# Performance work log

Hardware: AMD Instinct MI355X
Metric: run time of the kernel (lower is better)

## Reference

```python
import jax, jax.numpy as jnp
import numpy as np

DIM = 1024
HEADS = 16
HEAD_DIM = DIM // HEADS
BLOCK = 32
FEAT = 128
EPS = 1e-8


def setup_inputs() -> dict:
    key = jax.random.key(0)
    ks = jax.random.split(key, 5)
    b, n = 4, 4096
    x = jax.random.normal(ks[0], (b, n, DIM), dtype=jnp.float32)
    Wqkv = jax.random.normal(ks[1], (DIM, 3 * DIM), dtype=jnp.float32) / np.sqrt(DIM)
    proj = jax.random.normal(ks[2], (HEADS, HEAD_DIM, FEAT), dtype=jnp.float32) / np.sqrt(HEAD_DIM)
    Wout = jax.random.normal(ks[3], (DIM, DIM), dtype=jnp.float32) / np.sqrt(DIM)
    bout = jnp.zeros((DIM,), dtype=jnp.float32)
    return {"x": x, "Wqkv": Wqkv, "proj": proj, "Wout": Wout, "bout": bout}


def reference(x, Wqkv, proj, Wout, bout):
    b, n, d = x.shape
    h, dh = HEADS, HEAD_DIM
    nb = n // BLOCK
    qkv = x @ Wqkv                                    # [b, n, 3d]
    q, k, v = jnp.split(qkv, 3, axis=-1)
    # [b, h, nb, bs, dh]
    def to_blocks(t):
        return t.reshape(b, nb, BLOCK, h, dh).transpose(0, 3, 1, 2, 4)
    q, k, v = to_blocks(q), to_blocks(k), to_blocks(v)
    # per-head feature projection + elu feature map
    qf = jax.nn.elu(jnp.einsum('bhmsd,hdf->bhmsf', q, proj)) + 1.0
    kf = jax.nn.elu(jnp.einsum('bhmsd,hdf->bhmsf', k, proj)) + 1.0
    kv = jnp.einsum('bhmsf,bhmsd->bhmfd', kf, v)      # per-block kv state
    out = jnp.einsum('bhmsf,bhmfd->bhmsd', qf, kv)
    z = 1.0 / (jnp.einsum('bhmsf,bhmf->bhms', qf, kf.sum(axis=3)) + EPS)
    out = out * z[..., None]
    out = out.transpose(0, 2, 3, 1, 4).reshape(b, n, d)  # [b, n, d]
    return out @ Wout + bout
```

## Files before the change

### kernel.cpp

```cpp
#include <hip/hip_runtime.h>
#include <stdint.h>


typedef unsigned short u16;
typedef __attribute__((ext_vector_type(4))) float f32x4;
typedef __attribute__((ext_vector_type(8))) __bf16 bf16x8;
typedef __attribute__((ext_vector_type(8))) u16 us8;
typedef __attribute__((ext_vector_type(4))) u16 us4;

#define GLOAD_LDS16(g, l)                                                      \
  __builtin_amdgcn_global_load_lds(                                            \
      (const __attribute__((address_space(1))) void*)(g),                      \
      (__attribute__((address_space(3))) void*)(l), 16, 0, 0)

__device__ __forceinline__ u16 f2bf(float f) {
  union { float f; unsigned u; } x; x.f = f;
  return (u16)((x.u + 0x7fffu + ((x.u >> 16) & 1u)) >> 16);
}

__device__ __forceinline__ bf16x8 ld8(const void* p) {
  return __builtin_bit_cast(bf16x8, *(const us8*)p);
}

__device__ __forceinline__ f32x4 mfma16(bf16x8 a, bf16x8 b, f32x4 c) {
  return __builtin_amdgcn_mfma_f32_16x16x32_bf16(a, b, c, 0, 0, 0);
}

__global__ void cast_bf16_k(const float* __restrict__ in, u16* __restrict__ out,
                            int n4) {
  int stride = gridDim.x * blockDim.x;
  for (int i = blockIdx.x * blockDim.x + threadIdx.x; i < n4; i += stride) {
    f32x4 v = ((const f32x4*)in)[i];
    us4 o;
    o[0] = f2bf(v[0]); o[1] = f2bf(v[1]); o[2] = f2bf(v[2]); o[3] = f2bf(v[3]);
    ((us4*)out)[i] = o;
  }
}

__global__ __launch_bounds__(256)
void tcast_k(const float* __restrict__ in, u16* __restrict__ out, int R, int C) {
  __shared__ float tile[32][33];
  int tx = threadIdx.x & 31, ty = threadIdx.x >> 5;
  int r0 = blockIdx.y * 32, c0 = blockIdx.x * 32;
#pragma unroll
  for (int i = 0; i < 32; i += 8)
    tile[ty + i][tx] = in[(size_t)(r0 + ty + i) * C + c0 + tx];
  __syncthreads();
#pragma unroll
  for (int i = 0; i < 32; i += 8)
    out[(size_t)(c0 + ty + i) * R + r0 + tx] = f2bf(tile[tx][ty + i]);
}

__global__ void pcast_k(const float* __restrict__ in, u16* __restrict__ out) {
  int idx = blockIdx.x * 256 + threadIdx.x;
  int h = idx >> 13, f = (idx >> 6) & 127, e = idx & 63;
  out[idx] = f2bf(in[h * 8192 + e * 128 + f]);
}

template <bool OUTF32>
__global__ __launch_bounds__(256)
void gemm_bt(const u16* __restrict__ A, const u16* __restrict__ Bt,
             const float* __restrict__ bias, void* __restrict__ Cv,
             int M, int N, int K) {
  __shared__ __align__(16) u16 As[128 * 32];
  __shared__ __align__(16) u16 Bs[128 * 32];
  const int tid = threadIdx.x, lane = tid & 63, wave = tid >> 6;
  const int wr = wave >> 1, wc = wave & 1;
  const int bxN = blockIdx.x * 128;
  const int byM = blockIdx.y * 128;
  const int lr = lane & 15, lg = lane >> 4;
  const int r_in = lane >> 2;
  const int kch = (lane & 3) * 8;

  f32x4 acc[4][4];
#pragma unroll
  for (int m = 0; m < 4; ++m)
#pragma unroll
    for (int n = 0; n < 4; ++n) acc[m][n] = (f32x4){0.f, 0.f, 0.f, 0.f};

  for (int kt = 0; kt < K; kt += 32) {
    __syncthreads();
#pragma unroll
    for (int c = 0; c < 2; ++c) {
      int rowA = byM + wave * 32 + c * 16 + r_in;
      int rowB = bxN + wave * 32 + c * 16 + r_in;
      GLOAD_LDS16(A + (size_t)rowA * K + kt + kch, As + (wave * 2 + c) * 512);
      GLOAD_LDS16(Bt + (size_t)rowB * K + kt + kch, Bs + (wave * 2 + c) * 512);
    }
    __syncthreads();
    bf16x8 a[4], b[4];
#pragma unroll
    for (int m = 0; m < 4; ++m)
      a[m] = ld8(&As[(wr * 64 + m * 16 + lr) * 32 + lg * 8]);
#pragma unroll
    for (int n = 0; n < 4; ++n)
      b[n] = ld8(&Bs[(wc * 64 + n * 16 + lr) * 32 + lg * 8]);
#pragma unroll
    for (int m = 0; m < 4; ++m)
#pragma unroll
      for (int n = 0; n < 4; ++n) acc[m][n] = mfma16(a[m], b[n], acc[m][n]);
  }

  const int rbase = byM + wr * 64 + lg * 4;
  const int cbase = bxN + wc * 64 + lr;
#pragma unroll
  for (int m = 0; m < 4; ++m) {
#pragma unroll
    for (int n = 0; n < 4; ++n) {
      int col = cbase + n * 16;
      float bia = OUTF32 ? bias[col] : 0.f;
#pragma unroll
      for (int r = 0; r < 4; ++r) {
        int row = rbase + m * 16 + r;
        if (OUTF32)
          ((float*)Cv)[(size_t)row * N + col] = acc[m][n][r] + bia;
        else
          ((u16*)Cv)[(size_t)row * N + col] = f2bf(acc[m][n][r]);
      }
    }
  }
}

__global__ __launch_bounds__(64)
void attn_block_k(const u16* __restrict__ qkv, const u16* __restrict__ projT,
                  u16* __restrict__ attn) {
  __shared__ __align__(16) u16 qf_l[32 * 128];
  __shared__ __align__(16) u16 kf_l[32 * 128];
  __shared__ __align__(16) u16 V_l[32 * 72];
  __shared__ __align__(16) u16 S_l[32 * 32];

  const int lane = threadIdx.x;
  const int bid = blockIdx.x;
  const int m = bid & 127, h = (bid >> 7) & 15, b = bid >> 11;
  const size_t t0 = (size_t)b * 4096 + (size_t)m * 32;
  const u16* qb = qkv + t0 * 3072 + h * 64;
  const u16* kb = qb + 1024;
  const u16* vb = qb + 2048;
  const u16* pT = projT + h * 8192;
  const int lr = lane & 15, lg = lane >> 4;

  bf16x8 bp[8][2];
#pragma unroll
  for (int f = 0; f < 8; ++f)
#pragma unroll
    for (int ks = 0; ks < 2; ++ks)
      bp[f][ks] = ld8(&pT[(f * 16 + lr) * 64 + ks * 32 + lg * 8]);

#pragma unroll
  for (int it = 0; it < 4; ++it) {
    int s = it * 8 + (lane >> 3);
    int d0 = (lane & 7) * 8;
    *(us8*)&V_l[s * 72 + d0] = *(const us8*)&vb[(size_t)s * 3072 + d0];
  }

#pragma unroll
  for (int pass = 0; pass < 2; ++pass) {
    const u16* src = pass ? kb : qb;
    u16* dst = pass ? kf_l : qf_l;
    f32x4 acc[2][8];
#pragma unroll
    for (int mm = 0; mm < 2; ++mm)
#pragma unroll
      for (int f = 0; f < 8; ++f) acc[mm][f] = (f32x4){0.f, 0.f, 0.f, 0.f};
    bf16x8 afr[2][2];
#pragma unroll
    for (int mm = 0; mm < 2; ++mm)
#pragma unroll
      for (int ks = 0; ks < 2; ++ks)
        afr[mm][ks] = ld8(&src[(size_t)(mm * 16 + lr) * 3072 + ks * 32 + lg * 8]);
#pragma unroll
    for (int mm = 0; mm < 2; ++mm)
#pragma unroll
      for (int ks = 0; ks < 2; ++ks)
#pragma unroll
        for (int f = 0; f < 8; ++f)
          acc[mm][f] = mfma16(afr[mm][ks], bp[f][ks], acc[mm][f]);
#pragma unroll
    for (int mm = 0; mm < 2; ++mm)
#pragma unroll
      for (int f = 0; f < 8; ++f)
#pragma unroll
        for (int r = 0; r < 4; ++r) {
          float x = acc[mm][f][r];
          float v = x > 0.f ? x + 1.f : __expf(x);
          int row = mm * 16 + lg * 4 + r;
          int byi = (f * 16 + lr) * 2;
          *(u16*)((char*)dst + row * 256 + (byi ^ ((row & 7) << 4))) = f2bf(v);
        }
  }

  f32x4 sacc[2][2];
#pragma unroll
  for (int mm = 0; mm < 2; ++mm)
#pragma unroll
    for (int nn = 0; nn < 2; ++nn) sacc[mm][nn] = (f32x4){0.f, 0.f, 0.f, 0.f};
#pragma unroll
  for (int ks = 0; ks < 4; ++ks) {
    int byi = (ks * 32 + lg * 8) * 2;
    bf16x8 aq[2], bk[2];
#pragma unroll
    for (int mm = 0; mm < 2; ++mm) {
      int row = mm * 16 + lr;
      aq[mm] = ld8((char*)qf_l + row * 256 + (byi ^ ((row & 7) << 4)));
      bk[mm] = ld8((char*)kf_l + row * 256 + (byi ^ ((row & 7) << 4)));
    }
#pragma unroll
    for (int mm = 0; mm < 2; ++mm)
#pragma unroll
      for (int nn = 0; nn < 2; ++nn)
        sacc[mm][nn] = mfma16(aq[mm], bk[nn], sacc[mm][nn]);
  }

  float rs[2][4];
#pragma unroll
  for (int mm = 0; mm < 2; ++mm)
#pragma unroll
    for (int r = 0; r < 4; ++r) {
      float t = sacc[mm][0][r] + sacc[mm][1][r];
      t += __shfl_xor(t, 1);
      t += __shfl_xor(t, 2);
      t += __shfl_xor(t, 4);
      t += __shfl_xor(t, 8);
      rs[mm][r] = t;
    }

#pragma unroll
  for (int mm = 0; mm < 2; ++mm)
#pragma unroll
    for (int nn = 0; nn < 2; ++nn)
#pragma unroll
      for (int r = 0; r < 4; ++r) {
        int row = mm * 16 + lg * 4 + r;
        int byi = (nn * 16 + lr) * 2;
        *(u16*)((char*)S_l + row * 64 + (byi ^ ((row & 3) << 4))) =
            f2bf(sacc[mm][nn][r]);
      }

  bf16x8 vfr[4];
#pragma unroll
  for (int nn = 0; nn < 4; ++nn) {
    us8 g;
#pragma unroll
    for (int j = 0; j < 8; ++j) g[j] = V_l[(lg * 8 + j) * 72 + nn * 16 + lr];
    vfr[nn] = __builtin_bit_cast(bf16x8, g);
  }
  f32x4 pacc[2][4];
#pragma unroll
  for (int mm = 0; mm < 2; ++mm)
#pragma unroll
    for (int nn = 0; nn < 4; ++nn) pacc[mm][nn] = (f32x4){0.f, 0.f, 0.f, 0.f};
#pragma unroll
  for (int mm = 0; mm < 2; ++mm) {
    int row = mm * 16 + lr;
    int byi = lg * 16;
    bf16x8 a = ld8((char*)S_l + row * 64 + (byi ^ ((row & 3) << 4)));
#pragma unroll
    for (int nn = 0; nn < 4; ++nn) pacc[mm][nn] = mfma16(a, vfr[nn], pacc[mm][nn]);
  }

#pragma unroll
  for (int mm = 0; mm < 2; ++mm)
#pragma unroll
    for (int r = 0; r < 4; ++r) {
      float z = 1.f / (rs[mm][r] + 1e-8f);
      int q = mm * 16 + lg * 4 + r;
#pragma unroll
      for (int nn = 0; nn < 4; ++nn)
        attn[(t0 + q) * 1024 + h * 64 + nn * 16 + lr] =
            f2bf(pacc[mm][nn][r] * z);
    }
}

extern "C" void kernel_launch(void* const* d_in, const int* in_sizes, int n_in,
                              void* d_out, int out_size, void* d_ws,
                              size_t ws_size, hipStream_t stream) {
  const float* x = (const float*)d_in[0];
  const float* Wqkv = (const float*)d_in[1];
  const float* proj = (const float*)d_in[2];
  const float* Wout = (const float*)d_in[3];
  const float* bout = (const float*)d_in[4];
  float* out = (float*)d_out;

  char* ws = (char*)d_ws;
  u16* xb    = (u16*)(ws + 0);
  u16* wqkvT = (u16*)(ws + 33554432);
  u16* qkv   = (u16*)(ws + 39845888);
  u16* projT = (u16*)(ws + 140509184);
  u16* attn  = (u16*)(ws + 140771328);
  u16* woutT = (u16*)(ws + 174325760);

  cast_bf16_k<<<2048, 256, 0, stream>>>(x, xb, (16384 * 1024) / 4);
  tcast_k<<<dim3(3072 / 32, 1024 / 32), 256, 0, stream>>>(Wqkv, wqkvT, 1024, 3072);
  tcast_k<<<dim3(1024 / 32, 1024 / 32), 256, 0, stream>>>(Wout, woutT, 1024, 1024);
  pcast_k<<<512, 256, 0, stream>>>(proj, projT);

  gemm_bt<false><<<dim3(3072 / 128, 16384 / 128), 256, 0, stream>>>(
      xb, wqkvT, nullptr, qkv, 16384, 3072, 1024);

  attn_block_k<<<8192, 64, 0, stream>>>(qkv, projT, attn);

  gemm_bt<true><<<dim3(1024 / 128, 16384 / 128), 256, 0, stream>>>(
      attn, woutT, bout, out, 16384, 1024, 1024);
}
```

Measured before the change: 389.9 us.

## Fold feature projection into QKV weights and use 256x256 pipelined GEMM

Precomputes Wq·proj and Wk·proj on device so the first GEMM directly produces the 128-wide q/k features, with the elu+1 map applied in its epilogue. The attention kernel then only does the block-local score and value products, reading features from global memory. Both GEMMs switch to a 512-thread, 256x256-tile kernel with double-buffered LDS, a swizzled layout, and interleaved loads and MFMAs. This widens the first GEMM's N from 3072 to 5120, adding FLOPs, and uses the output buffer as scratch for the staged inputs.

```diff
diff --git a/kernel.cpp b/kernel.cpp
--- a/kernel.cpp
+++ b/kernel.cpp
@@ -51,142 +51,236 @@
     out[(size_t)(c0 + ty + i) * R + r0 + tx] = f2bf(tile[tx][ty + i]);
 }
 
-__global__ void pcast_k(const float* __restrict__ in, u16* __restrict__ out) {
-  int idx = blockIdx.x * 256 + threadIdx.x;
-  int h = idx >> 13, f = (idx >> 6) & 127, e = idx & 63;
-  out[idx] = f2bf(in[h * 8192 + e * 128 + f]);
-}
-
-template <bool OUTF32>
 __global__ __launch_bounds__(256)
-void gemm_bt(const u16* __restrict__ A, const u16* __restrict__ Bt,
-             const float* __restrict__ bias, void* __restrict__ Cv,
-             int M, int N, int K) {
-  __shared__ __align__(16) u16 As[128 * 32];
-  __shared__ __align__(16) u16 Bs[128 * 32];
-  const int tid = threadIdx.x, lane = tid & 63, wave = tid >> 6;
-  const int wr = wave >> 1, wc = wave & 1;
-  const int bxN = blockIdx.x * 128;
-  const int byM = blockIdx.y * 128;
+void tcastv_k(const float* __restrict__ Wqkv, u16* __restrict__ dst) {
+  __shared__ float tile[32][33];
+  int tx = threadIdx.x & 31, ty = threadIdx.x >> 5;
+  int e0 = blockIdx.y * 32, j0 = blockIdx.x * 32;
+#pragma unroll
+  for (int i = 0; i < 32; i += 8)
+    tile[ty + i][tx] = Wqkv[(size_t)(e0 + ty + i) * 3072 + 2048 + j0 + tx];
+  __syncthreads();
+#pragma unroll
+  for (int i = 0; i < 32; i += 8)
+    dst[(size_t)(j0 + ty + i) * 1024 + e0 + tx] = f2bf(tile[tx][ty + i]);
+}
+
+__global__ __launch_bounds__(256)
+void wqpb_k(const float* __restrict__ Wqkv, const float* __restrict__ proj,
+            u16* __restrict__ BtAll) {
+  __shared__ float pl[64][128];
+  const int ec = blockIdx.x, h = blockIdx.y, qk = blockIdx.z;
+  const float* ph = proj + (size_t)h * 8192;
+  for (int i = threadIdx.x; i < 2048; i += 256)
+    ((f32x4*)&pl[0][0])[i] = ((const f32x4*)ph)[i];
+  __syncthreads();
+  const int e = ec * 128 + (threadIdx.x >> 1);
+  const int f0 = (threadIdx.x & 1) * 64;
+  float wrow[64];
+  const float* src = Wqkv + (size_t)e * 3072 + qk * 1024 + h * 64;
+#pragma unroll
+  for (int i = 0; i < 16; ++i)
+    *(f32x4*)&wrow[i * 4] = *(const f32x4*)&src[i * 4];
+  u16* dst = BtAll + (size_t)(qk * 2048 + h * 128) * 1024 + e;
+  for (int fg = 0; fg < 16; ++fg) {
+    f32x4 acc = (f32x4){0.f, 0.f, 0.f, 0.f};
+    const int f = f0 + fg * 4;
+#pragma unroll
+    for (int d = 0; d < 64; ++d) {
+      f32x4 p = *(f32x4*)&pl[d][f];
+      acc += wrow[d] * p;
+    }
+#pragma unroll
+    for (int u = 0; u < 4; ++u) dst[(size_t)(f + u) * 1024] = f2bf(acc[u]);
+  }
+}
+
+template <int EPI>
+__global__ __launch_bounds__(512, 1)
+void gemm8p_k(const u16* __restrict__ A, int lda,
+              const u16* __restrict__ Bt, int ldb,
+              const float* __restrict__ bias,
+              u16* __restrict__ o_qkf, u16* __restrict__ o_v,
+              float* __restrict__ o_f32, int K, int ntx) {
+  __shared__ __align__(16) char lds[131072];
+  const int tid = threadIdx.x, lane = tid & 63, w = tid >> 6;
+  const int wm = w >> 2, wn = w & 3;
   const int lr = lane & 15, lg = lane >> 4;
-  const int r_in = lane >> 2;
-  const int kch = (lane & 3) * 8;
-
-  f32x4 acc[4][4];
-#pragma unroll
-  for (int m = 0; m < 4; ++m)
-#pragma unroll
-    for (int n = 0; n < 4; ++n) acc[m][n] = (f32x4){0.f, 0.f, 0.f, 0.f};
-
-  for (int kt = 0; kt < K; kt += 32) {
-    __syncthreads();
-#pragma unroll
-    for (int c = 0; c < 2; ++c) {
-      int rowA = byM + wave * 32 + c * 16 + r_in;
-      int rowB = bxN + wave * 32 + c * 16 + r_in;
-      GLOAD_LDS16(A + (size_t)rowA * K + kt + kch, As + (wave * 2 + c) * 512);
-      GLOAD_LDS16(Bt + (size_t)rowB * K + kt + kch, Bs + (wave * 2 + c) * 512);
-    }
-    __syncthreads();
-    bf16x8 a[4], b[4];
-#pragma unroll
-    for (int m = 0; m < 4; ++m)
-      a[m] = ld8(&As[(wr * 64 + m * 16 + lr) * 32 + lg * 8]);
-#pragma unroll
-    for (int n = 0; n < 4; ++n)
-      b[n] = ld8(&Bs[(wc * 64 + n * 16 + lr) * 32 + lg * 8]);
-#pragma unroll
-    for (int m = 0; m < 4; ++m)
-#pragma unroll
-      for (int n = 0; n < 4; ++n) acc[m][n] = mfma16(a[m], b[n], acc[m][n]);
-  }
-
-  const int rbase = byM + wr * 64 + lg * 4;
-  const int cbase = bxN + wc * 64 + lr;
-#pragma unroll
-  for (int m = 0; m < 4; ++m) {
-#pragma unroll
-    for (int n = 0; n < 4; ++n) {
-      int col = cbase + n * 16;
-      float bia = OUTF32 ? bias[col] : 0.f;
-#pragma unroll
-      for (int r = 0; r < 4; ++r) {
-        int row = rbase + m * 16 + r;
-        if (OUTF32)
-          ((float*)Cv)[(size_t)row * N + col] = acc[m][n][r] + bia;
-        else
-          ((u16*)Cv)[(size_t)row * N + col] = f2bf(acc[m][n][r]);
-      }
-    }
-  }
+  const int cpx = (int)gridDim.x >> 3;
+  const int bid = blockIdx.x;
+  const int s = (bid & 7) * cpx + (bid >> 3);
+  const int bxN = (s % ntx) * 256;
+  const int byM = (s / ntx) * 256;
+  const int nt = K >> 6;
+
+  const int srow = w * 8 + (lane >> 3);
+  const int scol = ((lane & 7) ^ ((lane >> 3) & 7)) * 8;
+
+  auto stg = [&](const u16* src, int ld, int row0, int kt, int dstoff) {
+#pragma unroll
+    for (int j = 0; j < 2; ++j)
+      GLOAD_LDS16(src + (size_t)(row0 + j * 64 + srow) * ld + kt + scol,
+                  lds + dstoff + j * 8192 + w * 1024);
+  };
+  auto stgA0 = [&](int t) { stg(A, lda, byM, t * 64, (t & 1) * 65536); };
+  auto stgA1 = [&](int t) { stg(A, lda, byM + 128, t * 64, (t & 1) * 65536 + 16384); };
+  auto stgB0 = [&](int t) { stg(Bt, ldb, bxN, t * 64, (t & 1) * 65536 + 32768); };
+  auto stgB1 = [&](int t) { stg(Bt, ldb, bxN + 128, t * 64, (t & 1) * 65536 + 49152); };
+
+  f32x4 acc[8][4];
+#pragma unroll
+  for (int i = 0; i < 8; ++i)
+#pragma unroll
+    for (int j = 0; j < 4; ++j) acc[i][j] = (f32x4){0.f, 0.f, 0.f, 0.f};
+
+  stgA0(0); stgA1(0); stgB0(0); stgB1(0);
+  if (nt > 1) {
+    stgB0(1); stgB1(1);
+    asm volatile("s_waitcnt vmcnt(4)" ::: "memory");
+  } else {
+    asm volatile("s_waitcnt vmcnt(0)" ::: "memory");
+  }
+  __builtin_amdgcn_s_barrier();
+
+  for (int t = 0; t < nt; ++t) {
+    const char* Ab = lds + (t & 1) * 65536 + wm * 16384;
+    const char* Bb = lds + (t & 1) * 65536 + 32768 + (wn >> 1) * 16384;
+    const int brow = (wn & 1) * 64;
+    bf16x8 a2[4][2], b2[4][2];
+
+#pragma unroll
+    for (int i = 0; i < 4; ++i)
+#pragma unroll
+      for (int ks = 0; ks < 2; ++ks) {
+        int row = i * 16 + lr;
+        a2[i][ks] = ld8(Ab + row * 128 + ((ks * 64 + lg * 16) ^ ((row & 7) << 4)));
+      }
+#pragma unroll
+    for (int j = 0; j < 2; ++j)
+#pragma unroll
+      for (int ks = 0; ks < 2; ++ks) {
+        int row = brow + j * 16 + lr;
+        b2[j][ks] = ld8(Bb + row * 128 + ((ks * 64 + lg * 16) ^ ((row & 7) << 4)));
+      }
+    if (t + 1 < nt) stgA0(t + 1);
+    __builtin_amdgcn_s_barrier();
+    asm volatile("s_waitcnt lgkmcnt(0)" ::: "memory");
+    __builtin_amdgcn_sched_barrier(0);
+    __builtin_amdgcn_s_setprio(1);
+#pragma unroll
+    for (int i = 0; i < 4; ++i)
+#pragma unroll
+      for (int j = 0; j < 2; ++j)
+#pragma unroll
+        for (int ks = 0; ks < 2; ++ks)
+          acc[i][j] = mfma16(a2[i][ks], b2[j][ks], acc[i][j]);
+    __builtin_amdgcn_s_setprio(0);
+    __builtin_amdgcn_s_barrier();
+
+#pragma unroll
+    for (int j = 2; j < 4; ++j)
+#pragma unroll
+      for (int ks = 0; ks < 2; ++ks) {
+        int row = brow + j * 16 + lr;
+        b2[j][ks] = ld8(Bb + row * 128 + ((ks * 64 + lg * 16) ^ ((row & 7) << 4)));
+      }
+    if (t + 1 < nt) stgA1(t + 1);
+    __builtin_amdgcn_s_barrier();
+    asm volatile("s_waitcnt lgkmcnt(0)" ::: "memory");
+    __builtin_amdgcn_sched_barrier(0);
+    __builtin_amdgcn_s_setprio(1);
+#pragma unroll
+    for (int i = 0; i < 4; ++i)
+#pragma unroll
+      for (int j = 2; j < 4; ++j)
+#pragma unroll
+        for (int ks = 0; ks < 2; ++ks)
+          acc[i][j] = mfma16(a2[i][ks], b2[j][ks], acc[i][j]);
+    __builtin_amdgcn_s_setprio(0);
+    __builtin_amdgcn_s_barrier();
+
+#pragma unroll
+    for (int i = 0; i < 4; ++i)
+#pragma unroll
+      for (int ks = 0; ks < 2; ++ks) {
+        int row = (4 + i) * 16 + lr;
+        a2[i][ks] = ld8(Ab + row * 128 + ((ks * 64 + lg * 16) ^ ((row & 7) << 4)));
+      }
+    if (t + 2 < nt) stgB0(t + 2);
+    __builtin_amdgcn_s_barrier();
+    asm volatile("s_waitcnt lgkmcnt(0)" ::: "memory");
+    __builtin_amdgcn_sched_barrier(0);
+    __builtin_amdgcn_s_setprio(1);
+#pragma unroll
+    for (int i = 0; i < 4; ++i)
+#pragma unroll
+      for (int j = 0; j < 2; ++j)
+#pragma unroll
+        for (int ks = 0; ks < 2; ++ks)
+          acc[4 + i][j] = mfma16(a2[i][ks], b2[j][ks], acc[4 + i][j]);
+    __builtin_amdgcn_s_setprio(0);
+    __builtin_amdgcn_s_barrier();
+
+    if (t + 2 < nt) stgB1(t + 2);
+    if (t < nt - 2)
+      asm volatile("s_waitcnt vmcnt(4)" ::: "memory");
+    else
+      asm volatile("s_waitcnt vmcnt(0)" ::: "memory");
+    __builtin_amdgcn_s_barrier();
+    __builtin_amdgcn_s_setprio(1);
+#pragma unroll
+    for (int i = 0; i < 4; ++i)
+#pragma unroll
+      for (int j = 2; j < 4; ++j)
+#pragma unroll
+        for (int ks = 0; ks < 2; ++ks)
+          acc[4 + i][j] = mfma16(a2[i][ks], b2[j][ks], acc[4 + i][j]);
+    __builtin_amdgcn_s_setprio(0);
+    __builtin_amdgcn_s_barrier();
+  }
+
+  const bool doelu = (EPI == 0) && (bxN < 4096);
+#pragma unroll
+  for (int mi = 0; mi < 8; ++mi)
+#pragma unroll
+    for (int nj = 0; nj < 4; ++nj) {
+      const int col = bxN + wn * 64 + nj * 16 + lr;
+#pragma unroll
+      for (int rr = 0; rr < 4; ++rr) {
+        const int row = byM + wm * 128 + mi * 16 + lg * 4 + rr;
+        float x = acc[mi][nj][rr];
+        if (EPI == 0) {
+          if (doelu) {
+            float v = x > 0.f ? x + 1.f : __expf(x);
+            o_qkf[(size_t)row * 4096 + col] = f2bf(v);
+          } else {
+            o_v[(size_t)row * 1024 + (col - 4096)] = f2bf(x);
+          }
+        } else {
+          o_f32[(size_t)row * 1024 + col] = x + bias[col];
+        }
+      }
+    }
 }
 
 __global__ __launch_bounds__(64)
-void attn_block_k(const u16* __restrict__ qkv, const u16* __restrict__ projT,
-                  u16* __restrict__ attn) {
-  __shared__ __align__(16) u16 qf_l[32 * 128];
-  __shared__ __align__(16) u16 kf_l[32 * 128];
+void attn_lite_k(const u16* __restrict__ qkf, u16* __restrict__ vbuf) {
   __shared__ __align__(16) u16 V_l[32 * 72];
   __shared__ __align__(16) u16 S_l[32 * 32];
-
   const int lane = threadIdx.x;
   const int bid = blockIdx.x;
   const int m = bid & 127, h = (bid >> 7) & 15, b = bid >> 11;
   const size_t t0 = (size_t)b * 4096 + (size_t)m * 32;
-  const u16* qb = qkv + t0 * 3072 + h * 64;
-  const u16* kb = qb + 1024;
-  const u16* vb = qb + 2048;
-  const u16* pT = projT + h * 8192;
+  const u16* qf = qkf + t0 * 4096 + h * 128;
+  const u16* kf = qf + 2048;
+  u16* vv = vbuf + t0 * 1024 + h * 64;
   const int lr = lane & 15, lg = lane >> 4;
 
-  bf16x8 bp[8][2];
-#pragma unroll
-  for (int f = 0; f < 8; ++f)
-#pragma unroll
-    for (int ks = 0; ks < 2; ++ks)
-      bp[f][ks] = ld8(&pT[(f * 16 + lr) * 64 + ks * 32 + lg * 8]);
-
 #pragma unroll
   for (int it = 0; it < 4; ++it) {
-    int s = it * 8 + (lane >> 3);
+    int s2 = it * 8 + (lane >> 3);
     int d0 = (lane & 7) * 8;
-    *(us8*)&V_l[s * 72 + d0] = *(const us8*)&vb[(size_t)s * 3072 + d0];
-  }
-
-#pragma unroll
-  for (int pass = 0; pass < 2; ++pass) {
-    const u16* src = pass ? kb : qb;
-    u16* dst = pass ? kf_l : qf_l;
-    f32x4 acc[2][8];
-#pragma unroll
-    for (int mm = 0; mm < 2; ++mm)
-#pragma unroll
-      for (int f = 0; f < 8; ++f) acc[mm][f] = (f32x4){0.f, 0.f, 0.f, 0.f};
-    bf16x8 afr[2][2];
-#pragma unroll
-    for (int mm = 0; mm < 2; ++mm)
-#pragma unroll
-      for (int ks = 0; ks < 2; ++ks)
-        afr[mm][ks] = ld8(&src[(size_t)(mm * 16 + lr) * 3072 + ks * 32 + lg * 8]);
-#pragma unroll
-    for (int mm = 0; mm < 2; ++mm)
-#pragma unroll
-      for (int ks = 0; ks < 2; ++ks)
-#pragma unroll
-        for (int f = 0; f < 8; ++f)
-          acc[mm][f] = mfma16(afr[mm][ks], bp[f][ks], acc[mm][f]);
-#pragma unroll
-    for (int mm = 0; mm < 2; ++mm)
-#pragma unroll
-      for (int f = 0; f < 8; ++f)
-#pragma unroll
-        for (int r = 0; r < 4; ++r) {
-          float x = acc[mm][f][r];
-          float v = x > 0.f ? x + 1.f : __expf(x);
-          int row = mm * 16 + lg * 4 + r;
-          int byi = (f * 16 + lr) * 2;
-          *(u16*)((char*)dst + row * 256 + (byi ^ ((row & 7) << 4))) = f2bf(v);
-        }
+    *(us8*)&V_l[s2 * 72 + d0] = *(const us8*)&vv[(size_t)s2 * 1024 + d0];
   }
 
   f32x4 sacc[2][2];
@@ -196,13 +290,11 @@
     for (int nn = 0; nn < 2; ++nn) sacc[mm][nn] = (f32x4){0.f, 0.f, 0.f, 0.f};
 #pragma unroll
   for (int ks = 0; ks < 4; ++ks) {
-    int byi = (ks * 32 + lg * 8) * 2;
     bf16x8 aq[2], bk[2];
 #pragma unroll
     for (int mm = 0; mm < 2; ++mm) {
-      int row = mm * 16 + lr;
-      aq[mm] = ld8((char*)qf_l + row * 256 + (byi ^ ((row & 7) << 4)));
-      bk[mm] = ld8((char*)kf_l + row * 256 + (byi ^ ((row & 7) << 4)));
+      aq[mm] = ld8(&qf[(size_t)(mm * 16 + lr) * 4096 + ks * 32 + lg * 8]);
+      bk[mm] = ld8(&kf[(size_t)(mm * 16 + lr) * 4096 + ks * 32 + lg * 8]);
     }
 #pragma unroll
     for (int mm = 0; mm < 2; ++mm)
@@ -266,8 +358,7 @@
       int q = mm * 16 + lg * 4 + r;
 #pragma unroll
       for (int nn = 0; nn < 4; ++nn)
-        attn[(t0 + q) * 1024 + h * 64 + nn * 16 + lr] =
-            f2bf(pacc[mm][nn][r] * z);
+        vv[(size_t)q * 1024 + nn * 16 + lr] = f2bf(pacc[mm][nn][r] * z);
     }
 }
 
@@ -282,23 +373,24 @@
   float* out = (float*)d_out;
 
   char* ws = (char*)d_ws;
-  u16* xb    = (u16*)(ws + 0);
-  u16* wqkvT = (u16*)(ws + 33554432);
-  u16* qkv   = (u16*)(ws + 39845888);
-  u16* projT = (u16*)(ws + 140509184);
-  u16* attn  = (u16*)(ws + 140771328);
-  u16* woutT = (u16*)(ws + 174325760);
-
-  cast_bf16_k<<<2048, 256, 0, stream>>>(x, xb, (16384 * 1024) / 4);
-  tcast_k<<<dim3(3072 / 32, 1024 / 32), 256, 0, stream>>>(Wqkv, wqkvT, 1024, 3072);
-  tcast_k<<<dim3(1024 / 32, 1024 / 32), 256, 0, stream>>>(Wout, woutT, 1024, 1024);
-  pcast_k<<<512, 256, 0, stream>>>(proj, projT);
-
-  gemm_bt<false><<<dim3(3072 / 128, 16384 / 128), 256, 0, stream>>>(
-      xb, wqkvT, nullptr, qkv, 16384, 3072, 1024);
-
-  attn_block_k<<<8192, 64, 0, stream>>>(qkv, projT, attn);
-
-  gemm_bt<true><<<dim3(1024 / 128, 16384 / 128), 256, 0, stream>>>(
-      attn, woutT, bout, out, 16384, 1024, 1024);
-}
+  char* doc = (char*)d_out;
+
+  u16* xb    = (u16*)doc;
+  u16* btall = (u16*)(doc + 33554432);
+  u16* qkf   = (u16*)ws;
+  u16* vbuf  = (u16*)(ws + 134217728);
+  u16* woutT = (u16*)(ws + 167772160);
+
+  cast_bf16_k<<<2048, 256, 0, stream>>>(x, xb, 4194304);
+  tcastv_k<<<dim3(32, 32), 256, 0, stream>>>(Wqkv, btall + (size_t)4096 * 1024);
+  wqpb_k<<<dim3(8, 16, 2), 256, 0, stream>>>(Wqkv, proj, btall);
+  tcast_k<<<dim3(32, 32), 256, 0, stream>>>(Wout, woutT, 1024, 1024);
+
+  gemm8p_k<0><<<1280, 512, 0, stream>>>(xb, 1024, btall, 1024, nullptr,
+                                        qkf, vbuf, nullptr, 1024, 20);
+
+  attn_lite_k<<<8192, 64, 0, stream>>>(qkf, vbuf);
+
+  gemm8p_k<1><<<256, 512, 0, stream>>>(vbuf, 1024, woutT, 1024, bout,
+                                       nullptr, nullptr, out, 1024, 4);
+}
```

After: 427.3 us. 1.1x slower.
